# Performance work log

Measured on AMD Instinct MI355X. Metric: run time of the kernel, lower is better.

The kernel has to match this reference:

```python
import jax, jax.numpy as jnp
import numpy as np

NUM_IN, IN_DIM, NUM_OUT, OUT_DIM, NUM_ROUTING = 1152, 8, 10, 16, 3
BATCH = 256


def squash(v):
    # v: (..., d). scale = |v|^2/(1+|v|^2) * v/|v|
    sq = jnp.sum(v * v, axis=-1, keepdims=True)
    scale = sq / (1.0 + sq)
    return scale * v / jnp.sqrt(sq + 1e-8)


def setup_inputs() -> dict:
    key = jax.random.key(0)
    k1, k2 = jax.random.split(key)
    input_capsules = jax.random.normal(k1, (BATCH, NUM_IN, IN_DIM), dtype=jnp.float32)
    W = jax.random.normal(k2, (NUM_IN, IN_DIM, NUM_OUT, OUT_DIM), dtype=jnp.float32) * 0.01
    return {"input_capsules": input_capsules, "W": W}


def reference(input_capsules, W):
    # u_hat: (b, i, j, o) -- predictions from each input capsule i for output capsule j
    u_hat = jnp.einsum('bid,idjo->bijo', input_capsules, W)
    b = jnp.zeros(u_hat.shape[:3] + (1,), dtype=u_hat.dtype)  # (b, i, j, 1)
    v = None
    for it in range(NUM_ROUTING):
        c = jax.nn.softmax(b, axis=2)                 # coupling coeffs over output capsules j
        s = jnp.sum(c * u_hat, axis=1)                # (b, j, o)
        v = squash(s)                                 # (b, j, o)
        if it < NUM_ROUTING - 1:
            agreement = jnp.sum(u_hat * v[:, None, :, :], axis=-1, keepdims=True)
            b = b + agreement
    return v
```

## Files before the change

kernel.cpp:

```cpp
#include <hip/hip_runtime.h>


#define NUM_IN 1152
#define NUM_OUT 10
#define OUT_DIM 16
#define BATCH 256
#define SLOTS 160
#define ICH_BLK 16
#define NCHUNK (NUM_IN / ICH_BLK)
#define BPB 16
#define NBT (BATCH / BPB)
#define WROW 1280

typedef unsigned int __attribute__((address_space(1))) as1_uint;
typedef unsigned int __attribute__((address_space(3))) as3_uint;
typedef int v2i __attribute__((ext_vector_type(2)));
typedef __fp16 h2 __attribute__((ext_vector_type(2)));
typedef float f2 __attribute__((ext_vector_type(2)));

#define PK_FMA_LO(acc, w, xp)                                         \
  asm("v_pk_fma_f32 %0, %1, %2, %0 op_sel:[0,0,0] op_sel_hi:[1,0,1]" \
      : "+v"(acc)                                                     \
      : "v"(w), "v"(xp))
#define PK_FMA_HI(acc, w, xp)                                         \
  asm("v_pk_fma_f32 %0, %1, %2, %0 op_sel:[0,1,0] op_sel_hi:[1,1,1]" \
      : "+v"(acc)                                                     \
      : "v"(w), "v"(xp))

__device__ __forceinline__ void gll16(const float* g, float* l) {
  __builtin_amdgcn_global_load_lds((const as1_uint*)g, (as3_uint*)l, 16, 0, 0);
}

__device__ __forceinline__ float xor8_sum(float x) {
  int v = __builtin_amdgcn_update_dpp(0, __float_as_int(x), 0x128, 0xF, 0xF, true);
  return x + __int_as_float(v);
}

__device__ __forceinline__ float xor32_sum(float x) {
  v2i r = __builtin_amdgcn_permlane32_swap(__float_as_int(x),
                                           __float_as_int(x), false, false);
  return __int_as_float(r.x) + __int_as_float(r.y);
}

__device__ __forceinline__ float rowsum8_hi(float x) {
  int v;
  v = __builtin_amdgcn_update_dpp(0, __float_as_int(x), 0x114, 0xF, 0xF, true);
  x += __int_as_float(v);
  v = __builtin_amdgcn_update_dpp(0, __float_as_int(x), 0x112, 0xF, 0xF, true);
  x += __int_as_float(v);
  v = __builtin_amdgcn_update_dpp(0, __float_as_int(x), 0x111, 0xF, 0xF, true);
  x += __int_as_float(v);
  return x;
}

__device__ __forceinline__ float rowsum16(float x) {
  int v;
  v = __builtin_amdgcn_update_dpp(0, __float_as_int(x), 0x128, 0xF, 0xF, true);
  x += __int_as_float(v);
  v = __builtin_amdgcn_update_dpp(0, __float_as_int(x), 0x124, 0xF, 0xF, true);
  x += __int_as_float(v);
  v = __builtin_amdgcn_update_dpp(0, __float_as_int(x), 0x122, 0xF, 0xF, true);
  x += __int_as_float(v);
  v = __builtin_amdgcn_update_dpp(0, __float_as_int(x), 0x121, 0xF, 0xF, true);
  x += __int_as_float(v);
  return x;
}

template <int PASS, int R, bool PART>
__device__ __forceinline__ void compute_round(
    const float* __restrict__ x, const float* __restrict__ v0p,
    const float* __restrict__ v1p, float* __restrict__ outp, const float* Wb,
    int i, int b0, int lane, int vbase, size_t obase) {
  constexpr size_t BBS = PART ? (size_t)(NCHUNK * SLOTS) : (size_t)SLOTS;
  const float* wsl = Wb + lane * 4;

  f2 xp[2][4];
#pragma unroll
  for (int bb = 0; bb < 2; ++bb) {
    const float* px = x + ((size_t)(b0 + bb) * NUM_IN + i) * 8;
    const float4 a = *reinterpret_cast<const float4*>(px);
    const float4 c = *reinterpret_cast<const float4*>(px + 4);
    xp[bb][0] = f2{a.x, a.y};
    xp[bb][1] = f2{a.z, a.w};
    xp[bb][2] = f2{c.x, c.y};
    xp[bb][3] = f2{c.z, c.w};
  }

  float cw[2][5];
  h2 up[2][5][2];

  if (PASS >= 1) {
#pragma unroll
    for (int jl = 0; jl < 5; ++jl) {
      f2 a0_01 = {0.f, 0.f}, a0_23 = {0.f, 0.f};
      f2 a1_01 = {0.f, 0.f}, a1_23 = {0.f, 0.f};
#pragma unroll
      for (int dp = 0; dp < 4; ++dp) {
        const float4 wA =
            *reinterpret_cast<const float4*>(wsl + ((2 * dp) * 5 + jl) * 256);
        const float4 wB = *reinterpret_cast<const float4*>(
            wsl + ((2 * dp + 1) * 5 + jl) * 256);
        const f2 wA01 = f2{wA.x, wA.y}, wA23 = f2{wA.z, wA.w};
        const f2 wB01 = f2{wB.x, wB.y}, wB23 = f2{wB.z, wB.w};
        PK_FMA_LO(a0_01, wA01, xp[0][dp]);
        PK_FMA_LO(a0_23, wA23, xp[0][dp]);
        PK_FMA_HI(a0_01, wB01, xp[0][dp]);
        PK_FMA_HI(a0_23, wB23, xp[0][dp]);
        PK_FMA_LO(a1_01, wA01, xp[1][dp]);
        PK_FMA_LO(a1_23, wA23, xp[1][dp]);
        PK_FMA_HI(a1_01, wB01, xp[1][dp]);
        PK_FMA_HI(a1_23, wB23, xp[1][dp]);
      }
      up[0][jl][0] = __builtin_amdgcn_cvt_pkrtz(a0_01.x, a0_01.y);
      up[0][jl][1] = __builtin_amdgcn_cvt_pkrtz(a0_23.x, a0_23.y);
      up[1][jl][0] = __builtin_amdgcn_cvt_pkrtz(a1_01.x, a1_01.y);
      up[1][jl][1] = __builtin_amdgcn_cvt_pkrtz(a1_23.x, a1_23.y);

      const float4 p0 = *reinterpret_cast<const float4*>(
          v0p + (b0 + 0) * SLOTS + vbase + jl * 16);
      const float4 p1 = *reinterpret_cast<const float4*>(
          v0p + (b0 + 1) * SLOTS + vbase + jl * 16);
      f2 t0 = a0_01 * f2{p0.x, p0.y} + a0_23 * f2{p0.z, p0.w};
      f2 t1 = a1_01 * f2{p1.x, p1.y} + a1_23 * f2{p1.z, p1.w};
      if (PASS == 2) {
        const float4 q0 = *reinterpret_cast<const float4*>(
            v1p + (b0 + 0) * SLOTS + vbase + jl * 16);
        const float4 q1 = *reinterpret_cast<const float4*>(
            v1p + (b0 + 1) * SLOTS + vbase + jl * 16);
        t0 += a0_01 * f2{q0.x, q0.y} + a0_23 * f2{q0.z, q0.w};
        t1 += a1_01 * f2{q1.x, q1.y} + a1_23 * f2{q1.z, q1.w};
      }
      cw[0][jl] = xor32_sum(xor8_sum(t0.x + t0.y));
      cw[1][jl] = xor32_sum(xor8_sum(t1.x + t1.y));
    }
#pragma unroll
    for (int bb = 0; bb < 2; ++bb) {
      float m = cw[bb][0];
#pragma unroll
      for (int jl = 1; jl < 5; ++jl) m = fmaxf(m, cw[bb][jl]);
      m = fmaxf(m, __shfl_xor(m, 16));
      float z = 0.f;
#pragma unroll
      for (int jl = 0; jl < 5; ++jl) {
        cw[bb][jl] = __expf(cw[bb][jl] - m);
        z += cw[bb][jl];
      }
      z += __shfl_xor(z, 16);
      const float rz = 1.0f / z;
#pragma unroll
      for (int jl = 0; jl < 5; ++jl) cw[bb][jl] *= rz;
    }
  }

  const bool wr = ((lane & 7) == 7);
#pragma unroll
  for (int jl = 0; jl < 5; ++jl) {
    float u0[4], u1[4];
    if (PASS == 0) {
      f2 a0_01 = {0.f, 0.f}, a0_23 = {0.f, 0.f};
      f2 a1_01 = {0.f, 0.f}, a1_23 = {0.f, 0.f};
#pragma unroll
      for (int dp = 0; dp < 4; ++dp) {
        const float4 wA =
            *reinterpret_cast<const float4*>(wsl + ((2 * dp) * 5 + jl) * 256);
        const float4 wB = *reinterpret_cast<const float4*>(
            wsl + ((2 * dp + 1) * 5 + jl) * 256);
        const f2 wA01 = f2{wA.x, wA.y}, wA23 = f2{wA.z, wA.w};
        const f2 wB01 = f2{wB.x, wB.y}, wB23 = f2{wB.z, wB.w};
        PK_FMA_LO(a0_01, wA01, xp[0][dp]);
        PK_FMA_LO(a0_23, wA23, xp[0][dp]);
        PK_FMA_HI(a0_01, wB01, xp[0][dp]);
        PK_FMA_HI(a0_23, wB23, xp[0][dp]);
        PK_FMA_LO(a1_01, wA01, xp[1][dp]);
        PK_FMA_LO(a1_23, wA23, xp[1][dp]);
        PK_FMA_HI(a1_01, wB01, xp[1][dp]);
        PK_FMA_HI(a1_23, wB23, xp[1][dp]);
      }
      u0[0] = a0_01.x * 0.1f; u0[1] = a0_01.y * 0.1f;
      u0[2] = a0_23.x * 0.1f; u0[3] = a0_23.y * 0.1f;
      u1[0] = a1_01.x * 0.1f; u1[1] = a1_01.y * 0.1f;
      u1[2] = a1_23.x * 0.1f; u1[3] = a1_23.y * 0.1f;
    } else {
      u0[0] = cw[0][jl] * (float)up[0][jl][0].x;
      u0[1] = cw[0][jl] * (float)up[0][jl][0].y;
      u0[2] = cw[0][jl] * (float)up[0][jl][1].x;
      u0[3] = cw[0][jl] * (float)up[0][jl][1].y;
      u1[0] = cw[1][jl] * (float)up[1][jl][0].x;
      u1[1] = cw[1][jl] * (float)up[1][jl][0].y;
      u1[2] = cw[1][jl] * (float)up[1][jl][1].x;
      u1[3] = cw[1][jl] * (float)up[1][jl][1].y;
    }
    const float sx0 = rowsum8_hi(u0[0]);
    const float sy0 = rowsum8_hi(u0[1]);
    const float sz0 = rowsum8_hi(u0[2]);
    const float sw0 = rowsum8_hi(u0[3]);
    const float sx1 = rowsum8_hi(u1[0]);
    const float sy1 = rowsum8_hi(u1[1]);
    const float sz1 = rowsum8_hi(u1[2]);
    const float sw1 = rowsum8_hi(u1[3]);
    if (wr) {
      if (PART) {
        float4* q0 = reinterpret_cast<float4*>(outp + obase + 0 * BBS + jl * 16);
        float4* q1 = reinterpret_cast<float4*>(outp + obase + 1 * BBS + jl * 16);
        float4 f0 = {sx0, sy0, sz0, sw0};
        float4 f1 = {sx1, sy1, sz1, sw1};
        if (R == 1) {
          const float4 o0 = *q0, o1 = *q1;
          f0.x += o0.x; f0.y += o0.y; f0.z += o0.z; f0.w += o0.w;
          f1.x += o1.x; f1.y += o1.y; f1.z += o1.z; f1.w += o1.w;
        }
        *q0 = f0;
        *q1 = f1;
      } else {
        float* p0 = outp + obase + 0 * BBS + jl * 16;
        float* p1 = outp + obase + 1 * BBS + jl * 16;
        atomicAdd(p0 + 0, sx0); atomicAdd(p0 + 1, sy0);
        atomicAdd(p0 + 2, sz0); atomicAdd(p0 + 3, sw0);
        atomicAdd(p1 + 0, sx1); atomicAdd(p1 + 1, sy1);
        atomicAdd(p1 + 2, sz1); atomicAdd(p1 + 3, sw1);
      }
    }
  }
}

template <int PASS, bool PART>
__global__ __launch_bounds__(512, 3) void caps_pass(
    const float* __restrict__ x, const float* __restrict__ W,
    const float* __restrict__ v0, const float* __restrict__ v1,
    float* __restrict__ outp) {
  __shared__ float Ws[10240];

  const int t = threadIdx.x;
  const int ic = blockIdx.x % NCHUNK;
  const int bt = blockIdx.x / NCHUNK;
  const int i0 = ic * ICH_BLK;

  const int lane = t & 63;
  const int wave = t >> 6;
  const int i_sub = lane & 7;
  const int oq = ((lane >> 3) & 1) | ((lane >> 4) & 2);
  const int jg = (lane >> 4) & 1;
  const int b0 = bt * BPB + wave * 2;
  const int vbase = jg * 80 + oq * 4;
  const size_t obase = PART ? ((size_t)b0 * NCHUNK + ic) * SLOTS + vbase
                            : (size_t)b0 * SLOTS + vbase;

  const float* wg = W + (size_t)i0 * WROW;

#pragma unroll
  for (int k = 0; k < 5; ++k) {
    const int p = t + k * 512;
    const int lp = p & 63;
    const int dj = p >> 6;
    const int d = dj / 5, jl = dj - d * 5;
    const int g = (lp & 7) * 320 + d * 40 + jl * 4 + ((lp >> 4) & 1) * 20 +
                  ((lp >> 3) & 1) + ((lp >> 5) & 1) * 2;
    gll16(wg + g * 4, &Ws[p * 4]);
  }
  asm volatile("s_waitcnt vmcnt(0)" ::: "memory");
  __builtin_amdgcn_s_barrier();

  compute_round<PASS, 0, PART>(x, v0, v1, outp, Ws, i0 + i_sub, b0, lane,
                               vbase, obase);

  asm volatile("s_waitcnt lgkmcnt(0)" ::: "memory");
  __builtin_amdgcn_s_barrier();

#pragma unroll
  for (int k = 0; k < 5; ++k) {
    const int p = t + k * 512;
    const int lp = p & 63;
    const int dj = p >> 6;
    const int d = dj / 5, jl = dj - d * 5;
    const int g = (lp & 7) * 320 + d * 40 + jl * 4 + ((lp >> 4) & 1) * 20 +
                  ((lp >> 3) & 1) + ((lp >> 5) & 1) * 2;
    gll16(wg + 8 * WROW + g * 4, &Ws[p * 4]);
  }
  asm volatile("s_waitcnt vmcnt(0)" ::: "memory");
  __builtin_amdgcn_s_barrier();

  compute_round<PASS, 1, PART>(x, v0, v1, outp, Ws, i0 + 8 + i_sub, b0, lane,
                               vbase, obase);
}

__global__ __launch_bounds__(192) void caps_reduce_squash(
    const float* __restrict__ part, float* __restrict__ v_out) {
  const int b = blockIdx.x;
  const int t = threadIdx.x;
  if (t < SLOTS) {
    const float* pb = part + (size_t)b * NCHUNK * SLOTS + t;
    float sv = 0.0f;
#pragma unroll 8
    for (int ic = 0; ic < NCHUNK; ++ic) sv += pb[ic * SLOTS];
    const float sq = rowsum16(sv * sv);
    const float scale = sq / (1.0f + sq) * rsqrtf(sq + 1e-8f);
    v_out[(size_t)b * SLOTS + t] = sv * scale;
  }
}

__global__ __launch_bounds__(192) void caps_squash(const float* s_in,
                                                   float* v_out,
                                                   float* s_zero) {
  const int b = blockIdx.x;
  const int t = threadIdx.x;
  if (t < SLOTS) {
    const float sv = s_in[(size_t)b * SLOTS + t];
    const float sq = rowsum16(sv * sv);
    const float scale = sq / (1.0f + sq) * rsqrtf(sq + 1e-8f);
    v_out[(size_t)b * SLOTS + t] = sv * scale;
    if (s_zero) s_zero[(size_t)b * SLOTS + t] = 0.0f;
  }
}

extern "C" void kernel_launch(void* const* d_in, const int* in_sizes, int n_in,
                              void* d_out, int out_size, void* d_ws,
                              size_t ws_size, hipStream_t stream) {
  const float* x = (const float*)d_in[0];
  const float* W = (const float*)d_in[1];
  float* out = (float*)d_out;

  const size_t part_elems = (size_t)NCHUNK * BATCH * SLOTS;
  const size_t need = (part_elems + 2 * BATCH * SLOTS) * sizeof(float);
  const dim3 pg(NCHUNK * NBT);

  if (ws_size >= need) {
    float* part = (float*)d_ws;
    float* v0 = part + part_elems;
    float* v1 = v0 + BATCH * SLOTS;
    caps_pass<0, true><<<pg, 512, 0, stream>>>(x, W, nullptr, nullptr, part);
    caps_reduce_squash<<<BATCH, 192, 0, stream>>>(part, v0);
    caps_pass<1, true><<<pg, 512, 0, stream>>>(x, W, v0, nullptr, part);
    caps_reduce_squash<<<BATCH, 192, 0, stream>>>(part, v1);
    caps_pass<2, true><<<pg, 512, 0, stream>>>(x, W, v0, v1, part);
    caps_reduce_squash<<<BATCH, 192, 0, stream>>>(part, out);
  } else {
    float* s_buf = (float*)d_ws;
    float* v0 = s_buf + BATCH * SLOTS;
    float* v1 = v0 + BATCH * SLOTS;
    hipMemsetAsync(s_buf, 0, (size_t)BATCH * SLOTS * sizeof(float), stream);
    caps_pass<0, false><<<pg, 512, 0, stream>>>(x, W, nullptr, nullptr, s_buf);
    caps_squash<<<BATCH, 192, 0, stream>>>(s_buf, v0, s_buf);
    caps_pass<1, false><<<pg, 512, 0, stream>>>(x, W, v0, nullptr, s_buf);
    caps_squash<<<BATCH, 192, 0, stream>>>(s_buf, v1, s_buf);
    caps_pass<2, false><<<pg, 512, 0, stream>>>(x, W, v0, v1, s_buf);
    caps_squash<<<BATCH, 192, 0, stream>>>(s_buf, out, nullptr);
  }
}
```

Measured before the change: 195.2 us.

## Split compute into LDS-read and reduce phases, overlap second W load with reduction

```diff
diff --git a/kernel.cpp b/kernel.cpp
--- a/kernel.cpp
+++ b/kernel.cpp
@@ -18,13 +18,13 @@
 typedef __fp16 h2 __attribute__((ext_vector_type(2)));
 typedef float f2 __attribute__((ext_vector_type(2)));
 
-#define PK_FMA_LO(acc, w, xp)                                         \
+#define PK_FMA_LO(acc, w, xp)                                        \
   asm("v_pk_fma_f32 %0, %1, %2, %0 op_sel:[0,0,0] op_sel_hi:[1,0,1]" \
-      : "+v"(acc)                                                     \
+      : "+v"(acc)                                                    \
       : "v"(w), "v"(xp))
-#define PK_FMA_HI(acc, w, xp)                                         \
+#define PK_FMA_HI(acc, w, xp)                                        \
   asm("v_pk_fma_f32 %0, %1, %2, %0 op_sel:[0,1,0] op_sel_hi:[1,1,1]" \
-      : "+v"(acc)                                                     \
+      : "+v"(acc)                                                    \
       : "v"(w), "v"(xp))
 
 __device__ __forceinline__ void gll16(const float* g, float* l) {
@@ -66,12 +66,13 @@
   return x;
 }
 
-template <int PASS, int R, bool PART>
-__device__ __forceinline__ void compute_round(
-    const float* __restrict__ x, const float* __restrict__ v0p,
-    const float* __restrict__ v1p, float* __restrict__ outp, const float* Wb,
-    int i, int b0, int lane, int vbase, size_t obase) {
-  constexpr size_t BBS = PART ? (size_t)(NCHUNK * SLOTS) : (size_t)SLOTS;
+template <int PASS>
+__device__ __forceinline__ void phase_A(const float* __restrict__ x,
+                                        const float* __restrict__ v0p,
+                                        const float* __restrict__ v1p,
+                                        const float* Wb, int i, int b0,
+                                        int lane, int vbase, float cw[2][5],
+                                        h2 up[2][5][2]) {
   const float* wsl = Wb + lane * 4;
 
   f2 xp[2][4];
@@ -86,36 +87,33 @@
     xp[bb][3] = f2{c.z, c.w};
   }
 
-  float cw[2][5];
-  h2 up[2][5][2];
-
-  if (PASS >= 1) {
-#pragma unroll
-    for (int jl = 0; jl < 5; ++jl) {
-      f2 a0_01 = {0.f, 0.f}, a0_23 = {0.f, 0.f};
-      f2 a1_01 = {0.f, 0.f}, a1_23 = {0.f, 0.f};
-#pragma unroll
-      for (int dp = 0; dp < 4; ++dp) {
-        const float4 wA =
-            *reinterpret_cast<const float4*>(wsl + ((2 * dp) * 5 + jl) * 256);
-        const float4 wB = *reinterpret_cast<const float4*>(
-            wsl + ((2 * dp + 1) * 5 + jl) * 256);
-        const f2 wA01 = f2{wA.x, wA.y}, wA23 = f2{wA.z, wA.w};
-        const f2 wB01 = f2{wB.x, wB.y}, wB23 = f2{wB.z, wB.w};
-        PK_FMA_LO(a0_01, wA01, xp[0][dp]);
-        PK_FMA_LO(a0_23, wA23, xp[0][dp]);
-        PK_FMA_HI(a0_01, wB01, xp[0][dp]);
-        PK_FMA_HI(a0_23, wB23, xp[0][dp]);
-        PK_FMA_LO(a1_01, wA01, xp[1][dp]);
-        PK_FMA_LO(a1_23, wA23, xp[1][dp]);
-        PK_FMA_HI(a1_01, wB01, xp[1][dp]);
-        PK_FMA_HI(a1_23, wB23, xp[1][dp]);
-      }
-      up[0][jl][0] = __builtin_amdgcn_cvt_pkrtz(a0_01.x, a0_01.y);
-      up[0][jl][1] = __builtin_amdgcn_cvt_pkrtz(a0_23.x, a0_23.y);
-      up[1][jl][0] = __builtin_amdgcn_cvt_pkrtz(a1_01.x, a1_01.y);
-      up[1][jl][1] = __builtin_amdgcn_cvt_pkrtz(a1_23.x, a1_23.y);
-
+#pragma unroll
+  for (int jl = 0; jl < 5; ++jl) {
+    f2 a0_01 = {0.f, 0.f}, a0_23 = {0.f, 0.f};
+    f2 a1_01 = {0.f, 0.f}, a1_23 = {0.f, 0.f};
+#pragma unroll
+    for (int dp = 0; dp < 4; ++dp) {
+      const float4 wA =
+          *reinterpret_cast<const float4*>(wsl + ((2 * dp) * 5 + jl) * 256);
+      const float4 wB = *reinterpret_cast<const float4*>(
+          wsl + ((2 * dp + 1) * 5 + jl) * 256);
+      const f2 wA01 = f2{wA.x, wA.y}, wA23 = f2{wA.z, wA.w};
+      const f2 wB01 = f2{wB.x, wB.y}, wB23 = f2{wB.z, wB.w};
+      PK_FMA_LO(a0_01, wA01, xp[0][dp]);
+      PK_FMA_LO(a0_23, wA23, xp[0][dp]);
+      PK_FMA_HI(a0_01, wB01, xp[0][dp]);
+      PK_FMA_HI(a0_23, wB23, xp[0][dp]);
+      PK_FMA_LO(a1_01, wA01, xp[1][dp]);
+      PK_FMA_LO(a1_23, wA23, xp[1][dp]);
+      PK_FMA_HI(a1_01, wB01, xp[1][dp]);
+      PK_FMA_HI(a1_23, wB23, xp[1][dp]);
+    }
+    up[0][jl][0] = __builtin_amdgcn_cvt_pkrtz(a0_01.x, a0_01.y);
+    up[0][jl][1] = __builtin_amdgcn_cvt_pkrtz(a0_23.x, a0_23.y);
+    up[1][jl][0] = __builtin_amdgcn_cvt_pkrtz(a1_01.x, a1_01.y);
+    up[1][jl][1] = __builtin_amdgcn_cvt_pkrtz(a1_23.x, a1_23.y);
+
+    if (PASS >= 1) {
       const float4 p0 = *reinterpret_cast<const float4*>(
           v0p + (b0 + 0) * SLOTS + vbase + jl * 16);
       const float4 p1 = *reinterpret_cast<const float4*>(
@@ -133,6 +131,14 @@
       cw[0][jl] = xor32_sum(xor8_sum(t0.x + t0.y));
       cw[1][jl] = xor32_sum(xor8_sum(t1.x + t1.y));
     }
+  }
+
+  if (PASS == 0) {
+#pragma unroll
+    for (int bb = 0; bb < 2; ++bb)
+#pragma unroll
+      for (int jl = 0; jl < 5; ++jl) cw[bb][jl] = 0.1f;
+  } else {
 #pragma unroll
     for (int bb = 0; bb < 2; ++bb) {
       float m = cw[bb][0];
@@ -151,57 +157,31 @@
       for (int jl = 0; jl < 5; ++jl) cw[bb][jl] *= rz;
     }
   }
-
+}
+
+template <int R, bool PART>
+__device__ __forceinline__ void phase_C(float* __restrict__ outp,
+                                        const float cw[2][5],
+                                        const h2 up[2][5][2], int lane,
+                                        size_t obase) {
+  constexpr size_t BBS = PART ? (size_t)(NCHUNK * SLOTS) : (size_t)SLOTS;
   const bool wr = ((lane & 7) == 7);
 #pragma unroll
   for (int jl = 0; jl < 5; ++jl) {
-    float u0[4], u1[4];
-    if (PASS == 0) {
-      f2 a0_01 = {0.f, 0.f}, a0_23 = {0.f, 0.f};
-      f2 a1_01 = {0.f, 0.f}, a1_23 = {0.f, 0.f};
-#pragma unroll
-      for (int dp = 0; dp < 4; ++dp) {
-        const float4 wA =
-            *reinterpret_cast<const float4*>(wsl + ((2 * dp) * 5 + jl) * 256);
-        const float4 wB = *reinterpret_cast<const float4*>(
-            wsl + ((2 * dp + 1) * 5 + jl) * 256);
-        const f2 wA01 = f2{wA.x, wA.y}, wA23 = f2{wA.z, wA.w};
-        const f2 wB01 = f2{wB.x, wB.y}, wB23 = f2{wB.z, wB.w};
-        PK_FMA_LO(a0_01, wA01, xp[0][dp]);
-        PK_FMA_LO(a0_23, wA23, xp[0][dp]);
-        PK_FMA_HI(a0_01, wB01, xp[0][dp]);
-        PK_FMA_HI(a0_23, wB23, xp[0][dp]);
-        PK_FMA_LO(a1_01, wA01, xp[1][dp]);
-        PK_FMA_LO(a1_23, wA23, xp[1][dp]);
-        PK_FMA_HI(a1_01, wB01, xp[1][dp]);
-        PK_FMA_HI(a1_23, wB23, xp[1][dp]);
-      }
-      u0[0] = a0_01.x * 0.1f; u0[1] = a0_01.y * 0.1f;
-      u0[2] = a0_23.x * 0.1f; u0[3] = a0_23.y * 0.1f;
-      u1[0] = a1_01.x * 0.1f; u1[1] = a1_01.y * 0.1f;
-      u1[2] = a1_23.x * 0.1f; u1[3] = a1_23.y * 0.1f;
-    } else {
-      u0[0] = cw[0][jl] * (float)up[0][jl][0].x;
-      u0[1] = cw[0][jl] * (float)up[0][jl][0].y;
-      u0[2] = cw[0][jl] * (float)up[0][jl][1].x;
-      u0[3] = cw[0][jl] * (float)up[0][jl][1].y;
-      u1[0] = cw[1][jl] * (float)up[1][jl][0].x;
-      u1[1] = cw[1][jl] * (float)up[1][jl][0].y;
-      u1[2] = cw[1][jl] * (float)up[1][jl][1].x;
-      u1[3] = cw[1][jl] * (float)up[1][jl][1].y;
-    }
-    const float sx0 = rowsum8_hi(u0[0]);
-    const float sy0 = rowsum8_hi(u0[1]);
-    const float sz0 = rowsum8_hi(u0[2]);
-    const float sw0 = rowsum8_hi(u0[3]);
-    const float sx1 = rowsum8_hi(u1[0]);
-    const float sy1 = rowsum8_hi(u1[1]);
-    const float sz1 = rowsum8_hi(u1[2]);
-    const float sw1 = rowsum8_hi(u1[3]);
+    const float sx0 = rowsum8_hi(cw[0][jl] * (float)up[0][jl][0].x);
+    const float sy0 = rowsum8_hi(cw[0][jl] * (float)up[0][jl][0].y);
+    const float sz0 = rowsum8_hi(cw[0][jl] * (float)up[0][jl][1].x);
+    const float sw0 = rowsum8_hi(cw[0][jl] * (float)up[0][jl][1].y);
+    const float sx1 = rowsum8_hi(cw[1][jl] * (float)up[1][jl][0].x);
+    const float sy1 = rowsum8_hi(cw[1][jl] * (float)up[1][jl][0].y);
+    const float sz1 = rowsum8_hi(cw[1][jl] * (float)up[1][jl][1].x);
+    const float sw1 = rowsum8_hi(cw[1][jl] * (float)up[1][jl][1].y);
     if (wr) {
       if (PART) {
-        float4* q0 = reinterpret_cast<float4*>(outp + obase + 0 * BBS + jl * 16);
-        float4* q1 = reinterpret_cast<float4*>(outp + obase + 1 * BBS + jl * 16);
+        float4* q0 =
+            reinterpret_cast<float4*>(outp + obase + 0 * BBS + jl * 16);
+        float4* q1 =
+            reinterpret_cast<float4*>(outp + obase + 1 * BBS + jl * 16);
         float4 f0 = {sx0, sy0, sz0, sw0};
         float4 f1 = {sx1, sy1, sz1, sw1};
         if (R == 1) {
@@ -224,7 +204,7 @@
 }
 
 template <int PASS, bool PART>
-__global__ __launch_bounds__(512, 3) void caps_pass(
+__global__ __launch_bounds__(512, 4) void caps_pass(
     const float* __restrict__ x, const float* __restrict__ W,
     const float* __restrict__ v0, const float* __restrict__ v1,
     float* __restrict__ outp) {
@@ -260,8 +240,10 @@
   asm volatile("s_waitcnt vmcnt(0)" ::: "memory");
   __builtin_amdgcn_s_barrier();
 
-  compute_round<PASS, 0, PART>(x, v0, v1, outp, Ws, i0 + i_sub, b0, lane,
-                               vbase, obase);
+  float cw[2][5];
+  h2 up[2][5][2];
+
+  phase_A<PASS>(x, v0, v1, Ws, i0 + i_sub, b0, lane, vbase, cw, up);
 
   asm volatile("s_waitcnt lgkmcnt(0)" ::: "memory");
   __builtin_amdgcn_s_barrier();
@@ -276,11 +258,14 @@
                   ((lp >> 3) & 1) + ((lp >> 5) & 1) * 2;
     gll16(wg + 8 * WROW + g * 4, &Ws[p * 4]);
   }
+
+  phase_C<0, PART>(outp, cw, up, lane, obase);
+
   asm volatile("s_waitcnt vmcnt(0)" ::: "memory");
   __builtin_amdgcn_s_barrier();
 
-  compute_round<PASS, 1, PART>(x, v0, v1, outp, Ws, i0 + 8 + i_sub, b0, lane,
-                               vbase, obase);
+  phase_A<PASS>(x, v0, v1, Ws, i0 + 8 + i_sub, b0, lane, vbase, cw, up);
+  phase_C<1, PART>(outp, cw, up, lane, obase);
 }
 
 __global__ __launch_bounds__(192) void caps_reduce_squash(
```

Measured after the change: 191.5 us. No clear change (-1.9%).
